# Kernel optimization log

Hardware: AMD Instinct MI355X
Metric: run time of the kernel (lower is better)

Reference implementation:

```python
import jax, jax.numpy as jnp
import numpy as np

B, C, L, K = 4096, 32768, 8192, 64  # batch, num_classes, num neighbour lists, max neighbours


def setup_inputs() -> dict:
    key = jax.random.key(0)
    k0, k1, k2, k3, k4 = jax.random.split(key, 5)
    x = jax.random.normal(k0, (B, C), dtype=jnp.float32)
    y = jax.random.randint(k1, (B,), 0, C)
    # position[c] >= 0 -> index into neighbour table (cluster sample); < 0 -> instance sample
    position = jax.random.randint(k2, (C,), -1, L)
    neighbours = jax.random.randint(k3, (L, K), 0, C)          # padded ragged neighbour lists
    neighbour_mask = jax.random.uniform(k4, (L, K)) < 0.7       # validity mask for padding
    return {"x": x, "y": y, "position": position, "neighbours": neighbours,
            "neighbour_mask": neighbour_mask}


def reference(x, y, position, neighbours, neighbour_mask):
    batch_size = x.shape[0]
    preds = jax.nn.softmax(x, axis=1)                           # [B, C]
    pos_y = position[y]                                         # [B]
    is_cluster = pos_y >= 0                                     # [B] bool
    # probability at the own label (used by both branches)
    p_label = jnp.take_along_axis(preds, y[:, None], axis=1)[:, 0]  # [B]
    # ragged neighbour gather+sum, vectorized over the batch
    list_idx = jnp.where(is_cluster, pos_y, 0)                  # safe index for non-cluster rows
    nbr = neighbours[list_idx]                                  # [B, K]
    msk = neighbour_mask[list_idx].astype(preds.dtype)          # [B, K]
    p_nbr = jnp.take_along_axis(preds, nbr, axis=1)             # [B, K]
    neigh_sum = jnp.sum(p_nbr * msk, axis=1)                    # [B]
    l_cls = -jnp.sum(jnp.where(is_cluster, jnp.log(p_label + neigh_sum), 0.0))
    l_ins = -jnp.sum(jnp.where(is_cluster, 0.0, jnp.log(p_label)))
    return (l_ins + l_cls) / batch_size
```

## Files before the change

kernel.cpp:

```cpp
#include <hip/hip_runtime.h>
#include <hip/hip_bf16.h>
#include <math.h>

#define BB 4096
#define CC 32768
#define KK 64

__global__ __launch_bounds__(256) void row_loss_kernel(
    const float* __restrict__ x,
    const int* __restrict__ y,
    const int* __restrict__ position,
    const int* __restrict__ neighbours,
    const void* __restrict__ mask_raw,
    float* __restrict__ row_out) {
  const int b = blockIdx.x;
  const int t = threadIdx.x;
  const int lane = t & 63;
  const int wv = t >> 6;

  const float4* row = reinterpret_cast<const float4*>(x + (size_t)b * CC);

  float s = 0.f;
#pragma unroll 8
  for (int i = 0; i < 32; ++i) {
    float4 v = row[t + i * 256];
    s += (__expf(v.x) + __expf(v.y)) + (__expf(v.z) + __expf(v.w));
  }
  for (int off = 32; off; off >>= 1) s += __shfl_xor(s, off);

  __shared__ float ss[4];
  if (lane == 0) ss[wv] = s;
  __syncthreads();
  const float S = ss[0] + ss[1] + ss[2] + ss[3];

  if (wv == 0) {
    const int yb = y[b];
    const int p = position[yb];
    const float xy = x[(size_t)b * CC + yb];

    if (p < 0) {
      if (lane == 0) row_out[b] = xy - __logf(S);
    } else {
      const unsigned int* mw = reinterpret_cast<const unsigned int*>(mask_raw);
      const unsigned int w0 = mw[lane];
      const bool is_float = __ballot(w0 == 0x3F800000u) != 0ull;
      const bool is_byte  = !is_float && (__ballot(w0 > 1u) != 0ull);

      const size_t mi = (size_t)p * KK + lane;
      bool valid;
      if (is_float)      valid = reinterpret_cast<const float*>(mask_raw)[mi] != 0.f;
      else if (is_byte)  valid = reinterpret_cast<const unsigned char*>(mask_raw)[mi] != 0;
      else               valid = reinterpret_cast<const int*>(mask_raw)[mi] != 0;

      const int idx = neighbours[mi];
      float e = valid ? __expf(x[(size_t)b * CC + idx]) : 0.f;
      for (int off = 32; off; off >>= 1) e += __shfl_xor(e, off);
      if (lane == 0) row_out[b] = __logf(__expf(xy) + e) - __logf(S);
    }
  }
}

__global__ __launch_bounds__(256) void finalize_kernel(
    const float* __restrict__ row_out, float* __restrict__ out) {
  const int t = threadIdx.x;
  float acc = 0.f;
#pragma unroll
  for (int i = 0; i < BB / 256; ++i) acc += row_out[t + i * 256];
  for (int off = 32; off; off >>= 1) acc += __shfl_xor(acc, off);
  __shared__ float ws[4];
  if ((t & 63) == 0) ws[t >> 6] = acc;
  __syncthreads();
  if (t == 0) out[0] = -(ws[0] + ws[1] + ws[2] + ws[3]) / (float)BB;
}

extern "C" void kernel_launch(void* const* d_in, const int* in_sizes, int n_in,
                              void* d_out, int out_size, void* d_ws, size_t ws_size,
                              hipStream_t stream) {
  const float* x          = reinterpret_cast<const float*>(d_in[0]);
  const int*   y          = reinterpret_cast<const int*>(d_in[1]);
  const int*   position   = reinterpret_cast<const int*>(d_in[2]);
  const int*   neighbours = reinterpret_cast<const int*>(d_in[3]);
  const void*  mask       = d_in[4];
  float* out = reinterpret_cast<float*>(d_out);
  float* ws  = reinterpret_cast<float*>(d_ws);

  row_loss_kernel<<<BB, 256, 0, stream>>>(x, y, position, neighbours, mask, ws);
  finalize_kernel<<<1, 256, 0, stream>>>(ws, out);
}
```

Before: 98.81 us.

## Split each row's softmax denominator across eight blocks and combine in finalize

```diff
diff --git a/kernel.cpp b/kernel.cpp
--- a/kernel.cpp
+++ b/kernel.cpp
@@ -5,42 +5,49 @@
 #define BB 4096
 #define CC 32768
 #define KK 64
+#define CHUNKS 8
+#define NBLK1 (BB * CHUNKS)
 
-__global__ __launch_bounds__(256) void row_loss_kernel(
+__global__ __launch_bounds__(256) void chunk_sum_kernel(
     const float* __restrict__ x,
     const int* __restrict__ y,
     const int* __restrict__ position,
     const int* __restrict__ neighbours,
     const void* __restrict__ mask_raw,
-    float* __restrict__ row_out) {
+    float* __restrict__ partial,
+    float* __restrict__ e_out,
+    float* __restrict__ xy_out) {
   const int b = blockIdx.x;
+  const int r = b >> 3;
   const int t = threadIdx.x;
   const int lane = t & 63;
   const int wv = t >> 6;
+  const bool tail_block = (b & 7) == 0;
 
-  const float4* row = reinterpret_cast<const float4*>(x + (size_t)b * CC);
+  int p = -1;
+  float xy = 0.f;
+  if (tail_block) {
+    const int yb = y[r];
+    p = position[yb];
+    xy = x[(size_t)r * CC + yb];
+  }
 
+  const float4* p4 = reinterpret_cast<const float4*>(x) + (size_t)b * 1024 + t;
   float s = 0.f;
-#pragma unroll 8
-  for (int i = 0; i < 32; ++i) {
-    float4 v = row[t + i * 256];
+#pragma unroll
+  for (int i = 0; i < 4; ++i) {
+    float4 v = p4[i * 256];
     s += (__expf(v.x) + __expf(v.y)) + (__expf(v.z) + __expf(v.w));
   }
   for (int off = 32; off; off >>= 1) s += __shfl_xor(s, off);
-
   __shared__ float ss[4];
   if (lane == 0) ss[wv] = s;
   __syncthreads();
-  const float S = ss[0] + ss[1] + ss[2] + ss[3];
+  if (t == 0) partial[b] = ss[0] + ss[1] + ss[2] + ss[3];
 
-  if (wv == 0) {
-    const int yb = y[b];
-    const int p = position[yb];
-    const float xy = x[(size_t)b * CC + yb];
-
-    if (p < 0) {
-      if (lane == 0) row_out[b] = xy - __logf(S);
-    } else {
+  if (tail_block && wv == 0) {
+    float e = 0.f;
+    if (p >= 0) {
       const unsigned int* mw = reinterpret_cast<const unsigned int*>(mask_raw);
       const unsigned int w0 = mw[lane];
       const bool is_float = __ballot(w0 == 0x3F800000u) != 0ull;
@@ -53,24 +60,39 @@
       else               valid = reinterpret_cast<const int*>(mask_raw)[mi] != 0;
 
       const int idx = neighbours[mi];
-      float e = valid ? __expf(x[(size_t)b * CC + idx]) : 0.f;
-      for (int off = 32; off; off >>= 1) e += __shfl_xor(e, off);
-      if (lane == 0) row_out[b] = __logf(__expf(xy) + e) - __logf(S);
+      float ev = valid ? __expf(x[(size_t)r * CC + idx]) : 0.f;
+      for (int off = 32; off; off >>= 1) ev += __shfl_xor(ev, off);
+      e = ev;
     }
+    if (lane == 0) { e_out[r] = e; xy_out[r] = xy; }
   }
 }
 
-__global__ __launch_bounds__(256) void finalize_kernel(
-    const float* __restrict__ row_out, float* __restrict__ out) {
+__global__ __launch_bounds__(1024) void finalize_kernel(
+    const float* __restrict__ partial,
+    const float* __restrict__ e_in,
+    const float* __restrict__ xy_in,
+    float* __restrict__ out) {
   const int t = threadIdx.x;
   float acc = 0.f;
 #pragma unroll
-  for (int i = 0; i < BB / 256; ++i) acc += row_out[t + i * 256];
+  for (int i = 0; i < 4; ++i) {
+    const int r = t + i * 1024;
+    const float4* pp = reinterpret_cast<const float4*>(partial + r * CHUNKS);
+    const float4 a = pp[0], c = pp[1];
+    const float S = ((a.x + a.y) + (a.z + a.w)) + ((c.x + c.y) + (c.z + c.w));
+    acc += __logf(__expf(xy_in[r]) + e_in[r]) - __logf(S);
+  }
   for (int off = 32; off; off >>= 1) acc += __shfl_xor(acc, off);
-  __shared__ float ws[4];
+  __shared__ float ws[16];
   if ((t & 63) == 0) ws[t >> 6] = acc;
   __syncthreads();
-  if (t == 0) out[0] = -(ws[0] + ws[1] + ws[2] + ws[3]) / (float)BB;
+  if (t == 0) {
+    float tot = 0.f;
+#pragma unroll
+    for (int w = 0; w < 16; ++w) tot += ws[w];
+    out[0] = -tot / (float)BB;
+  }
 }
 
 extern "C" void kernel_launch(void* const* d_in, const int* in_sizes, int n_in,
@@ -82,8 +104,12 @@
   const int*   neighbours = reinterpret_cast<const int*>(d_in[3]);
   const void*  mask       = d_in[4];
   float* out = reinterpret_cast<float*>(d_out);
-  float* ws  = reinterpret_cast<float*>(d_ws);
 
-  row_loss_kernel<<<BB, 256, 0, stream>>>(x, y, position, neighbours, mask, ws);
-  finalize_kernel<<<1, 256, 0, stream>>>(ws, out);
+  float* partial = reinterpret_cast<float*>(d_ws);
+  float* e_buf   = partial + NBLK1;
+  float* xy_buf  = e_buf + BB;
+
+  chunk_sum_kernel<<<NBLK1, 256, 0, stream>>>(x, y, position, neighbours, mask,
+                                              partial, e_buf, xy_buf);
+  finalize_kernel<<<1, 1024, 0, stream>>>(partial, e_buf, xy_buf, out);
 }
```

New measurement: 104.5 us. 1.06x slower.
